# Performance work log

Measured on AMD Instinct MI355X. Metric: run time of the kernel, lower is better.

Reference implementation:

```python
import jax, jax.numpy as jnp
import numpy as np

T, B, D_IN, D_H, D_MID, D_OUT = 16, 16384, 64, 256, 64, 4


def setup_inputs() -> dict:
    key = jax.random.key(0)
    ks = jax.random.split(key, 12)
    s = 0.05
    return {
        "x": jax.random.normal(ks[0], (T, B, D_IN), dtype=jnp.float32),
        "hc1": jnp.zeros((B, D_H), dtype=jnp.float32),
        "W_i2h": jax.random.normal(ks[1], (D_H, D_IN), dtype=jnp.float32) * s,
        "b_i2h": jax.random.normal(ks[2], (D_H,), dtype=jnp.float32) * s,
        "W_h2h": jax.random.normal(ks[3], (D_H, D_H), dtype=jnp.float32) * s,
        "b_h2h": jax.random.normal(ks[4], (D_H,), dtype=jnp.float32) * s,
        "W_h2o": jax.random.normal(ks[5], (D_MID, D_H), dtype=jnp.float32) * s,
        "b_h2o": jax.random.normal(ks[6], (D_MID,), dtype=jnp.float32) * s,
        "W_fc": jax.random.normal(ks[7], (D_OUT, D_MID), dtype=jnp.float32) * s,
        "b_fc": jax.random.normal(ks[8], (D_OUT,), dtype=jnp.float32) * s,
    }


def reference(x, hc1, W_i2h, b_i2h, W_h2h, b_h2h, W_h2o, b_h2o, W_fc, b_fc):
    # 16-step vanilla RNN: h = tanh(i2h(x_t) + h2h(h)); out = fc(tanh(h2o(h)))
    def step(h, xt):
        h_new = jnp.tanh(xt @ W_i2h.T + b_i2h + h @ W_h2h.T + b_h2h)  # [B, 256]
        out = jnp.tanh(h_new @ W_h2o.T + b_h2o) @ W_fc.T + b_fc       # [B, 4]
        return h_new, out

    h_final, output_seq = jax.lax.scan(step, hc1, x)
    return output_seq, h_final
```

## Files before the change

kernel.cpp:

```cpp
#include <hip/hip_runtime.h>


typedef _Float16 half8 __attribute__((ext_vector_type(8)));
typedef float floatx4 __attribute__((ext_vector_type(4)));

#define T_STEPS  16
#define BATCH    16384
#define BLK_ROWS 32
#define HS       264
#define MS       72

__device__ inline float fast_tanh(float x) {
    float t = __builtin_amdgcn_exp2f(x * 2.8853900817779268f);
    return 1.0f - 2.0f * __builtin_amdgcn_rcpf(t + 1.0f);
}

__device__ inline half8 cvt8(const float* __restrict__ p) {
    float4 a = ((const float4*)p)[0];
    float4 b = ((const float4*)p)[1];
    half8 h;
    h[0] = (_Float16)a.x; h[1] = (_Float16)a.y; h[2] = (_Float16)a.z; h[3] = (_Float16)a.w;
    h[4] = (_Float16)b.x; h[5] = (_Float16)b.y; h[6] = (_Float16)b.z; h[7] = (_Float16)b.w;
    return h;
}

__global__ __launch_bounds__(256, 2) void rnn_kernel(
    const float* __restrict__ x,   const float* __restrict__ hc1,
    const float* __restrict__ Wi,  const float* __restrict__ bi,
    const float* __restrict__ Wh,  const float* __restrict__ bh,
    const float* __restrict__ Wo,  const float* __restrict__ bo,
    const float* __restrict__ Wf,  const float* __restrict__ bf,
    float* __restrict__ out)
{
    __shared__ _Float16 h_lds[BLK_ROWS * HS];
    __shared__ _Float16 mid_lds[BLK_ROWS * MS];
    __shared__ float    biasPre[256];
    __shared__ float    bo_lds[64];
    __shared__ _Float16 wfc_lds[4 * 64];
    __shared__ float    bfc_lds[4];

    const int tid  = threadIdx.x;
    const int w    = tid >> 6;
    const int lane = tid & 63;
    const int l16  = lane & 15;
    const int quad = lane >> 4;
    const int b0   = blockIdx.x * BLK_ROWS;

    biasPre[tid] = bi[tid] + bh[tid];
    if (tid < 64) bo_lds[tid] = bo[tid];
    wfc_lds[tid] = (_Float16)Wf[tid];
    if (tid < 4) bfc_lds[tid] = bf[tid];

    {
        int r = tid >> 3, c0 = (tid & 7) * 32;
        const float4* src = (const float4*)&hc1[(size_t)(b0 + r) * 256 + c0];
        #pragma unroll
        for (int i = 0; i < 8; ++i) {
            float4 v = src[i];
            int c = c0 + i * 4;
            h_lds[r * HS + c + 0] = (_Float16)v.x;
            h_lds[r * HS + c + 1] = (_Float16)v.y;
            h_lds[r * HS + c + 2] = (_Float16)v.z;
            h_lds[r * HS + c + 3] = (_Float16)v.w;
        }
    }

    half8 wcat[10][4];
    #pragma unroll
    for (int ks = 0; ks < 10; ++ks) {
        #pragma unroll
        for (int nt = 0; nt < 4; ++nt) {
            int j = w * 64 + nt * 16 + l16;
            const float* src = (ks < 2)
                ? (Wi + (size_t)j * 64  + ks * 32 + quad * 8)
                : (Wh + (size_t)j * 256 + (ks - 2) * 32 + quad * 8);
            wcat[ks][nt] = cvt8(src);
        }
    }
    half8 wof[8];
    #pragma unroll
    for (int ks = 0; ks < 8; ++ks) {
        int j = w * 16 + l16;
        wof[ks] = cvt8(Wo + (size_t)j * 256 + ks * 32 + quad * 8);
    }

    __syncthreads();

    for (int t = 0; t < T_STEPS; ++t) {
        half8 afx[2][2];
        #pragma unroll
        for (int mt = 0; mt < 2; ++mt) {
            int m = mt * 16 + l16;
            const float* xr = x + ((size_t)t * BATCH + b0 + m) * 64;
            #pragma unroll
            for (int k2 = 0; k2 < 2; ++k2)
                afx[mt][k2] = cvt8(xr + k2 * 32 + quad * 8);
        }

        floatx4 acc[2][4];
        #pragma unroll
        for (int mt = 0; mt < 2; ++mt)
            #pragma unroll
            for (int nt = 0; nt < 4; ++nt)
                acc[mt][nt] = (floatx4){0.f, 0.f, 0.f, 0.f};

        #pragma unroll
        for (int ks = 0; ks < 10; ++ks) {
            half8 af[2];
            #pragma unroll
            for (int mt = 0; mt < 2; ++mt) {
                if (ks < 2) {
                    af[mt] = afx[mt][ks];
                } else {
                    int m = mt * 16 + l16;
                    af[mt] = *(const half8*)&h_lds[m * HS + (ks - 2) * 32 + quad * 8];
                }
            }
            #pragma unroll
            for (int mt = 0; mt < 2; ++mt)
                #pragma unroll
                for (int nt = 0; nt < 4; ++nt)
                    acc[mt][nt] = __builtin_amdgcn_mfma_f32_16x16x32_f16(
                        af[mt], wcat[ks][nt], acc[mt][nt], 0, 0, 0);
        }

        __syncthreads();

        #pragma unroll
        for (int nt = 0; nt < 4; ++nt) {
            int col = w * 64 + nt * 16 + l16;
            float bias = biasPre[col];
            #pragma unroll
            for (int mt = 0; mt < 2; ++mt) {
                #pragma unroll
                for (int r = 0; r < 4; ++r) {
                    int row = mt * 16 + quad * 4 + r;
                    h_lds[row * HS + col] = (_Float16)fast_tanh(acc[mt][nt][r] + bias);
                }
            }
        }

        __syncthreads();

        floatx4 acc2[2];
        #pragma unroll
        for (int mt = 0; mt < 2; ++mt) acc2[mt] = (floatx4){0.f, 0.f, 0.f, 0.f};
        #pragma unroll
        for (int ks = 0; ks < 8; ++ks) {
            #pragma unroll
            for (int mt = 0; mt < 2; ++mt) {
                int m = mt * 16 + l16;
                half8 af = *(const half8*)&h_lds[m * HS + ks * 32 + quad * 8];
                acc2[mt] = __builtin_amdgcn_mfma_f32_16x16x32_f16(
                    af, wof[ks], acc2[mt], 0, 0, 0);
            }
        }
        {
            int col = w * 16 + l16;
            float bias = bo_lds[col];
            #pragma unroll
            for (int mt = 0; mt < 2; ++mt)
                #pragma unroll
                for (int r = 0; r < 4; ++r) {
                    int row = mt * 16 + quad * 4 + r;
                    mid_lds[row * MS + col] = (_Float16)fast_tanh(acc2[mt][r] + bias);
                }
        }

        __syncthreads();

        if (tid < 128) {
            int row = tid >> 2, oc = tid & 3;
            float s = bfc_lds[oc];
            #pragma unroll
            for (int k8 = 0; k8 < 64; k8 += 8) {
                half8 mv = *(const half8*)&mid_lds[row * MS + k8];
                half8 wv = *(const half8*)&wfc_lds[oc * 64 + k8];
                #pragma unroll
                for (int j = 0; j < 8; ++j)
                    s += (float)mv[j] * (float)wv[j];
            }
            out[((size_t)t * BATCH + b0 + row) * 4 + oc] = s;
        }
    }

    {
        int r = tid >> 3, c0 = (tid & 7) * 32;
        float4* dst = (float4*)&out[(size_t)T_STEPS * BATCH * 4 + (size_t)(b0 + r) * 256 + c0];
        #pragma unroll
        for (int i = 0; i < 8; ++i) {
            int c = c0 + i * 4;
            float4 v;
            v.x = (float)h_lds[r * HS + c + 0];
            v.y = (float)h_lds[r * HS + c + 1];
            v.z = (float)h_lds[r * HS + c + 2];
            v.w = (float)h_lds[r * HS + c + 3];
            dst[i] = v;
        }
    }
}

extern "C" void kernel_launch(void* const* d_in, const int* in_sizes, int n_in,
                              void* d_out, int out_size, void* d_ws, size_t ws_size,
                              hipStream_t stream) {
    const float* x   = (const float*)d_in[0];
    const float* hc1 = (const float*)d_in[1];
    const float* Wi  = (const float*)d_in[2];
    const float* bi  = (const float*)d_in[3];
    const float* Wh  = (const float*)d_in[4];
    const float* bh  = (const float*)d_in[5];
    const float* Wo  = (const float*)d_in[6];
    const float* bo  = (const float*)d_in[7];
    const float* Wf  = (const float*)d_in[8];
    const float* bf  = (const float*)d_in[9];

    rnn_kernel<<<BATCH / BLK_ROWS, 256, 0, stream>>>(
        x, hc1, Wi, bi, Wh, bh, Wo, bo, Wf, bf, (float*)d_out);
}
```

Baseline: 219.0 us.

## Software-pipeline RNN steps with double-buffered LDS and async x prefetch

Restructures the time loop so each step's h2h MFMAs share h fragment loads with the previous step's h2o MFMAs, and the fc output is deferred by one step. h, mid and x are double-buffered in LDS, with x prefetched via global_load_lds using an XOR swizzle. This cuts barriers per step from three to one and overlaps global x loads with compute. MFMA operand order is swapped so epilogue stores become vectorized half4 writes, and the fc dot product is split across thread pairs. It uses more LDS and adds pipeline prologue and epilogue complexity, which may lower occupancy.

```diff
diff --git a/kernel.cpp b/kernel.cpp
--- a/kernel.cpp
+++ b/kernel.cpp
@@ -2,6 +2,7 @@
 
 
 typedef _Float16 half8 __attribute__((ext_vector_type(8)));
+typedef _Float16 half4 __attribute__((ext_vector_type(4)));
 typedef float floatx4 __attribute__((ext_vector_type(4)));
 
 #define T_STEPS  16
@@ -10,18 +11,133 @@
 #define HS       264
 #define MS       72
 
+#define AS1C(p) ((const __attribute__((address_space(1))) unsigned int*)(p))
+#define AS3(p)  ((__attribute__((address_space(3))) unsigned int*)(p))
+
 __device__ inline float fast_tanh(float x) {
     float t = __builtin_amdgcn_exp2f(x * 2.8853900817779268f);
     return 1.0f - 2.0f * __builtin_amdgcn_rcpf(t + 1.0f);
 }
 
-__device__ inline half8 cvt8(const float* __restrict__ p) {
-    float4 a = ((const float4*)p)[0];
-    float4 b = ((const float4*)p)[1];
+__device__ inline half8 pack8(float4 a, float4 b) {
     half8 h;
     h[0] = (_Float16)a.x; h[1] = (_Float16)a.y; h[2] = (_Float16)a.z; h[3] = (_Float16)a.w;
     h[4] = (_Float16)b.x; h[5] = (_Float16)b.y; h[6] = (_Float16)b.z; h[7] = (_Float16)b.w;
     return h;
+}
+
+__device__ inline half8 cvt8(const float* __restrict__ p) {
+    return pack8(((const float4*)p)[0], ((const float4*)p)[1]);
+}
+
+template<int DO_PRE, int DO_MID>
+__device__ __forceinline__ void mfma_phase(
+    const _Float16* __restrict__ hcur, const float* __restrict__ xcur,
+    const half8 (&wcat)[10][4], const half8 (&wof)[8],
+    floatx4 (&acc)[2][4], floatx4 (&ac2)[2], int l16, int quad)
+{
+    #pragma unroll
+    for (int ks2 = 0; ks2 < 8; ++ks2) {
+        half8 hf[2];
+        #pragma unroll
+        for (int mt = 0; mt < 2; ++mt)
+            hf[mt] = *(const half8*)&hcur[(mt * 16 + l16) * HS + ks2 * 32 + quad * 8];
+        if (DO_PRE) {
+            #pragma unroll
+            for (int mt = 0; mt < 2; ++mt)
+                #pragma unroll
+                for (int nt = 0; nt < 4; ++nt)
+                    acc[mt][nt] = __builtin_amdgcn_mfma_f32_16x16x32_f16(
+                        wcat[ks2 + 2][nt], hf[mt], acc[mt][nt], 0, 0, 0);
+        }
+        if (DO_MID) {
+            #pragma unroll
+            for (int mt = 0; mt < 2; ++mt)
+                ac2[mt] = __builtin_amdgcn_mfma_f32_16x16x32_f16(
+                    wof[ks2], hf[mt], ac2[mt], 0, 0, 0);
+        }
+    }
+    if (DO_PRE) {
+        #pragma unroll
+        for (int k2 = 0; k2 < 2; ++k2) {
+            half8 af[2];
+            #pragma unroll
+            for (int mt = 0; mt < 2; ++mt) {
+                int row = mt * 16 + l16, sw = row & 7;
+                int ub = row * 16 + k2 * 8 + quad * 2;
+                float4 a = *(const float4*)&xcur[(ub ^ sw) * 4];
+                float4 b = *(const float4*)&xcur[((ub + 1) ^ sw) * 4];
+                af[mt] = pack8(a, b);
+            }
+            #pragma unroll
+            for (int mt = 0; mt < 2; ++mt)
+                #pragma unroll
+                for (int nt = 0; nt < 4; ++nt)
+                    acc[mt][nt] = __builtin_amdgcn_mfma_f32_16x16x32_f16(
+                        wcat[k2][nt], af[mt], acc[mt][nt], 0, 0, 0);
+        }
+    }
+}
+
+__device__ __forceinline__ void epi_h(_Float16* __restrict__ hnxt,
+                                      const floatx4 (&acc)[2][4],
+                                      const float* __restrict__ biasPre,
+                                      int w, int l16, int quad)
+{
+    #pragma unroll
+    for (int nt = 0; nt < 4; ++nt) {
+        int hb = w * 64 + nt * 16 + quad * 4;
+        float4 bias = *(const float4*)&biasPre[hb];
+        #pragma unroll
+        for (int mt = 0; mt < 2; ++mt) {
+            int mb = mt * 16 + l16;
+            half4 v;
+            v[0] = (_Float16)fast_tanh(acc[mt][nt][0] + bias.x);
+            v[1] = (_Float16)fast_tanh(acc[mt][nt][1] + bias.y);
+            v[2] = (_Float16)fast_tanh(acc[mt][nt][2] + bias.z);
+            v[3] = (_Float16)fast_tanh(acc[mt][nt][3] + bias.w);
+            *(half4*)&hnxt[mb * HS + hb] = v;
+        }
+    }
+}
+
+__device__ __forceinline__ void epi_mid(_Float16* __restrict__ midp,
+                                        const floatx4 (&ac2)[2],
+                                        const float* __restrict__ bo_lds,
+                                        int w, int l16, int quad)
+{
+    int md = w * 16 + quad * 4;
+    float4 bo4 = *(const float4*)&bo_lds[md];
+    #pragma unroll
+    for (int mt = 0; mt < 2; ++mt) {
+        int mb = mt * 16 + l16;
+        half4 v;
+        v[0] = (_Float16)fast_tanh(ac2[mt][0] + bo4.x);
+        v[1] = (_Float16)fast_tanh(ac2[mt][1] + bo4.y);
+        v[2] = (_Float16)fast_tanh(ac2[mt][2] + bo4.z);
+        v[3] = (_Float16)fast_tanh(ac2[mt][3] + bo4.w);
+        *(half4*)&midp[mb * MS + md] = v;
+    }
+}
+
+__device__ __forceinline__ void fc_out(const _Float16* __restrict__ midp,
+                                       const _Float16* __restrict__ wfc,
+                                       const float* __restrict__ bfc,
+                                       float* __restrict__ outp,
+                                       int ti, int b0, int tid)
+{
+    const int row = tid >> 3, oc = (tid >> 1) & 3, kh = tid & 1;
+    float s = 0.f;
+    #pragma unroll
+    for (int k8 = 0; k8 < 32; k8 += 8) {
+        half8 mv = *(const half8*)&midp[row * MS + kh * 32 + k8];
+        half8 wv = *(const half8*)&wfc[oc * 64 + kh * 32 + k8];
+        #pragma unroll
+        for (int j = 0; j < 8; ++j) s += (float)mv[j] * (float)wv[j];
+    }
+    s += __shfl_xor(s, 1, 64);
+    if (kh == 0)
+        outp[((size_t)ti * BATCH + b0 + row) * 4 + oc] = s + bfc[oc];
 }
 
 __global__ __launch_bounds__(256, 2) void rnn_kernel(
@@ -32,8 +148,9 @@
     const float* __restrict__ Wf,  const float* __restrict__ bf,
     float* __restrict__ out)
 {
-    __shared__ _Float16 h_lds[BLK_ROWS * HS];
-    __shared__ _Float16 mid_lds[BLK_ROWS * MS];
+    __shared__ _Float16 h_lds[2][BLK_ROWS * HS];
+    __shared__ float    x_lds[2][BLK_ROWS * 64];
+    __shared__ _Float16 mid_lds[2][BLK_ROWS * MS];
     __shared__ float    biasPre[256];
     __shared__ float    bo_lds[64];
     __shared__ _Float16 wfc_lds[4 * 64];
@@ -46,28 +163,50 @@
     const int quad = lane >> 4;
     const int b0   = blockIdx.x * BLK_ROWS;
 
+    const int g0 = tid ^ ((tid >> 4) & 7);
+    const int u1 = 256 + tid;
+    const int g1 = u1 ^ ((u1 >> 4) & 7);
+
+#define PREFETCH_X(ti, xb) do {                                                        \
+        const float* xsrc_ = x + ((size_t)(ti) * BATCH + b0) * 64;                     \
+        __builtin_amdgcn_global_load_lds(AS1C(xsrc_ + (size_t)g0 * 4),                 \
+                                         AS3(&x_lds[xb][w * 256]), 16, 0, 0);          \
+        __builtin_amdgcn_global_load_lds(AS1C(xsrc_ + (size_t)g1 * 4),                 \
+                                         AS3(&x_lds[xb][1024 + w * 256]), 16, 0, 0);   \
+    } while (0)
+
+#define ZERO_ACC() do {                                                                \
+        _Pragma("unroll")                                                              \
+        for (int mt = 0; mt < 2; ++mt) {                                               \
+            ac2[mt] = (floatx4){0.f, 0.f, 0.f, 0.f};                                   \
+            _Pragma("unroll")                                                          \
+            for (int nt = 0; nt < 4; ++nt) acc[mt][nt] = (floatx4){0.f, 0.f, 0.f, 0.f};\
+        }                                                                              \
+    } while (0)
+
+    PREFETCH_X(0, 0);
+
     biasPre[tid] = bi[tid] + bh[tid];
     if (tid < 64) bo_lds[tid] = bo[tid];
     wfc_lds[tid] = (_Float16)Wf[tid];
     if (tid < 4) bfc_lds[tid] = bf[tid];
 
     {
-        int r = tid >> 3, c0 = (tid & 7) * 32;
+        const int r = tid >> 3, c0 = (tid & 7) * 32;
         const float4* src = (const float4*)&hc1[(size_t)(b0 + r) * 256 + c0];
         #pragma unroll
-        for (int i = 0; i < 8; ++i) {
-            float4 v = src[i];
-            int c = c0 + i * 4;
-            h_lds[r * HS + c + 0] = (_Float16)v.x;
-            h_lds[r * HS + c + 1] = (_Float16)v.y;
-            h_lds[r * HS + c + 2] = (_Float16)v.z;
-            h_lds[r * HS + c + 3] = (_Float16)v.w;
+        for (int i2 = 0; i2 < 8; ++i2) {
+            float4 v = src[i2];
+            half4 hv;
+            hv[0] = (_Float16)v.x; hv[1] = (_Float16)v.y;
+            hv[2] = (_Float16)v.z; hv[3] = (_Float16)v.w;
+            *(half4*)&h_lds[0][r * HS + c0 + i2 * 4] = hv;
         }
     }
 
     half8 wcat[10][4];
     #pragma unroll
-    for (int ks = 0; ks < 10; ++ks) {
+    for (int ks = 0; ks < 10; ++ks)
         #pragma unroll
         for (int nt = 0; nt < 4; ++nt) {
             int j = w * 64 + nt * 16 + l16;
@@ -76,128 +215,61 @@
                 : (Wh + (size_t)j * 256 + (ks - 2) * 32 + quad * 8);
             wcat[ks][nt] = cvt8(src);
         }
-    }
     half8 wof[8];
     #pragma unroll
-    for (int ks = 0; ks < 8; ++ks) {
-        int j = w * 16 + l16;
-        wof[ks] = cvt8(Wo + (size_t)j * 256 + ks * 32 + quad * 8);
-    }
+    for (int ks = 0; ks < 8; ++ks)
+        wof[ks] = cvt8(Wo + (size_t)(w * 16 + l16) * 256 + ks * 32 + quad * 8);
 
     __syncthreads();
 
-    for (int t = 0; t < T_STEPS; ++t) {
-        half8 afx[2][2];
-        #pragma unroll
-        for (int mt = 0; mt < 2; ++mt) {
-            int m = mt * 16 + l16;
-            const float* xr = x + ((size_t)t * BATCH + b0 + m) * 64;
-            #pragma unroll
-            for (int k2 = 0; k2 < 2; ++k2)
-                afx[mt][k2] = cvt8(xr + k2 * 32 + quad * 8);
-        }
-
-        floatx4 acc[2][4];
-        #pragma unroll
-        for (int mt = 0; mt < 2; ++mt)
-            #pragma unroll
-            for (int nt = 0; nt < 4; ++nt)
-                acc[mt][nt] = (floatx4){0.f, 0.f, 0.f, 0.f};
-
-        #pragma unroll
-        for (int ks = 0; ks < 10; ++ks) {
-            half8 af[2];
-            #pragma unroll
-            for (int mt = 0; mt < 2; ++mt) {
-                if (ks < 2) {
-                    af[mt] = afx[mt][ks];
-                } else {
-                    int m = mt * 16 + l16;
-                    af[mt] = *(const half8*)&h_lds[m * HS + (ks - 2) * 32 + quad * 8];
-                }
-            }
-            #pragma unroll
-            for (int mt = 0; mt < 2; ++mt)
-                #pragma unroll
-                for (int nt = 0; nt < 4; ++nt)
-                    acc[mt][nt] = __builtin_amdgcn_mfma_f32_16x16x32_f16(
-                        af[mt], wcat[ks][nt], acc[mt][nt], 0, 0, 0);
-        }
-
+    {
+        PREFETCH_X(1, 1);
+        floatx4 acc[2][4], ac2[2];
+        ZERO_ACC();
+        mfma_phase<1, 0>(h_lds[0], x_lds[0], wcat, wof, acc, ac2, l16, quad);
+        epi_h(h_lds[1], acc, biasPre, w, l16, quad);
         __syncthreads();
-
-        #pragma unroll
-        for (int nt = 0; nt < 4; ++nt) {
-            int col = w * 64 + nt * 16 + l16;
-            float bias = biasPre[col];
-            #pragma unroll
-            for (int mt = 0; mt < 2; ++mt) {
-                #pragma unroll
-                for (int r = 0; r < 4; ++r) {
-                    int row = mt * 16 + quad * 4 + r;
-                    h_lds[row * HS + col] = (_Float16)fast_tanh(acc[mt][nt][r] + bias);
-                }
-            }
-        }
-
+    }
+
+    #pragma unroll 1
+    for (int i = 1; i <= 15; ++i) {
+        const int cur = i & 1, nxt = cur ^ 1;
+        if (i < 15) PREFETCH_X(i + 1, nxt);
+        if (i >= 2) fc_out(mid_lds[nxt], wfc_lds, bfc_lds, out, i - 2, b0, tid);
+        floatx4 acc[2][4], ac2[2];
+        ZERO_ACC();
+        mfma_phase<1, 1>(h_lds[cur], x_lds[cur], wcat, wof, acc, ac2, l16, quad);
+        epi_h(h_lds[nxt], acc, biasPre, w, l16, quad);
+        epi_mid(mid_lds[cur], ac2, bo_lds, w, l16, quad);
         __syncthreads();
-
-        floatx4 acc2[2];
-        #pragma unroll
-        for (int mt = 0; mt < 2; ++mt) acc2[mt] = (floatx4){0.f, 0.f, 0.f, 0.f};
-        #pragma unroll
-        for (int ks = 0; ks < 8; ++ks) {
-            #pragma unroll
-            for (int mt = 0; mt < 2; ++mt) {
-                int m = mt * 16 + l16;
-                half8 af = *(const half8*)&h_lds[m * HS + ks * 32 + quad * 8];
-                acc2[mt] = __builtin_amdgcn_mfma_f32_16x16x32_f16(
-                    af, wof[ks], acc2[mt], 0, 0, 0);
-            }
-        }
-        {
-            int col = w * 16 + l16;
-            float bias = bo_lds[col];
-            #pragma unroll
-            for (int mt = 0; mt < 2; ++mt)
-                #pragma unroll
-                for (int r = 0; r < 4; ++r) {
-                    int row = mt * 16 + quad * 4 + r;
-                    mid_lds[row * MS + col] = (_Float16)fast_tanh(acc2[mt][r] + bias);
-                }
-        }
-
+    }
+
+    {
+        fc_out(mid_lds[1], wfc_lds, bfc_lds, out, 14, b0, tid);
+        floatx4 acc[2][4], ac2[2];
+        ZERO_ACC();
+        mfma_phase<0, 1>(h_lds[0], x_lds[0], wcat, wof, acc, ac2, l16, quad);
+        epi_mid(mid_lds[0], ac2, bo_lds, w, l16, quad);
         __syncthreads();
-
-        if (tid < 128) {
-            int row = tid >> 2, oc = tid & 3;
-            float s = bfc_lds[oc];
-            #pragma unroll
-            for (int k8 = 0; k8 < 64; k8 += 8) {
-                half8 mv = *(const half8*)&mid_lds[row * MS + k8];
-                half8 wv = *(const half8*)&wfc_lds[oc * 64 + k8];
-                #pragma unroll
-                for (int j = 0; j < 8; ++j)
-                    s += (float)mv[j] * (float)wv[j];
-            }
-            out[((size_t)t * BATCH + b0 + row) * 4 + oc] = s;
-        }
-    }
-
-    {
-        int r = tid >> 3, c0 = (tid & 7) * 32;
+        fc_out(mid_lds[0], wfc_lds, bfc_lds, out, 15, b0, tid);
+    }
+
+    {
+        const int r = tid >> 3, c0 = (tid & 7) * 32;
         float4* dst = (float4*)&out[(size_t)T_STEPS * BATCH * 4 + (size_t)(b0 + r) * 256 + c0];
         #pragma unroll
-        for (int i = 0; i < 8; ++i) {
-            int c = c0 + i * 4;
+        for (int i2 = 0; i2 < 8; ++i2) {
+            int c = c0 + i2 * 4;
             float4 v;
-            v.x = (float)h_lds[r * HS + c + 0];
-            v.y = (float)h_lds[r * HS + c + 1];
-            v.z = (float)h_lds[r * HS + c + 2];
-            v.w = (float)h_lds[r * HS + c + 3];
-            dst[i] = v;
-        }
-    }
+            v.x = (float)h_lds[0][r * HS + c + 0];
+            v.y = (float)h_lds[0][r * HS + c + 1];
+            v.z = (float)h_lds[0][r * HS + c + 2];
+            v.w = (float)h_lds[0][r * HS + c + 3];
+            dst[i2] = v;
+        }
+    }
+#undef PREFETCH_X
+#undef ZERO_ACC
 }
 
 extern "C" void kernel_launch(void* const* d_in, const int* in_sizes, int n_in,
```

Measured after the change: 216.3 us. No clear change (-1.3%).
